# Performance work log

Hardware: AMD Instinct MI355X
Metric: run time of the kernel (lower is better)

Reference implementation:

```python
import jax, jax.numpy as jnp
import numpy as np

LEVELS = 16
FEATURES = 2
HASHMAP_SIZE = 524288
BASE_RES = 16
PER_LEVEL_SCALE = 1.3819

_P1, _P2, _P3 = np.uint32(73856093), np.uint32(19349663), np.uint32(83492791)
# 8 trilinear corner offsets, bit order (x, y, z)
_OFFSETS = np.array([[ox, oy, oz] for ox in (0, 1) for oy in (0, 1) for oz in (0, 1)], dtype=np.int32)


def setup_inputs() -> dict:
    key = jax.random.key(0)
    kx, kt = jax.random.split(key)
    x = jax.random.uniform(kx, (2000000, 3), dtype=jnp.float32)
    tables = jax.random.normal(kt, (LEVELS, HASHMAP_SIZE, FEATURES), dtype=jnp.float32) * 0.01
    return {"x": x, "tables": tables}


def _hash_coords(corners_u32):
    # corners_u32: [N, 8, 3] uint32; spatial hash with uint32 wraparound.
    h = (corners_u32[..., 0] * _P1) ^ (corners_u32[..., 1] * _P2) ^ (corners_u32[..., 2] * _P3)
    return (h % np.uint32(HASHMAP_SIZE)).astype(jnp.int32)  # [N, 8]


def _encode(x, tables):
    offsets_i = jnp.asarray(_OFFSETS)                 # [8, 3] int32
    offsets_f = offsets_i.astype(x.dtype)             # [8, 3]
    embeds = []
    for l in range(LEVELS):
        res = int(BASE_RES * PER_LEVEL_SCALE ** l)
        pos = x * res                                  # [N, 3]
        pos_floor = jnp.floor(pos)
        w = pos - pos_floor                            # [N, 3] trilinear weights
        base = pos_floor.astype(jnp.int32)             # non-negative (x in [0,1])
        corners = (base[:, None, :] + offsets_i).astype(jnp.uint32)  # [N, 8, 3]
        idx = _hash_coords(corners)                    # [N, 8]
        vals = tables[l][idx]                          # [N, 8, F] gather
        # weight per corner = prod over axes of (w if offset else 1-w)
        wgt = jnp.prod(offsets_f * w[:, None, :] + (1.0 - offsets_f) * (1.0 - w[:, None, :]), axis=-1)  # [N, 8]
        embeds.append(jnp.einsum('nc,ncf->nf', wgt, vals))  # [N, F]
    return jnp.concatenate(embeds, axis=-1)           # [N, LEVELS*F]


def reference(x, tables):
    return _encode(x, tables)
```

## Files before the change

### kernel.cpp

```cpp
#include <hip/hip_runtime.h>
#include <stdint.h>

#define LEVELS 16
#define FEAT 2
#define TABLE_SIZE 524288
#define TMASK (TABLE_SIZE - 1)

typedef float f32x2 __attribute__((ext_vector_type(2)));
typedef float f32x4 __attribute__((ext_vector_type(4)));
typedef float f32x4u __attribute__((ext_vector_type(4), aligned(8)));

__device__ __constant__ int kRes[LEVELS] = {
    16, 22, 30, 42, 58, 80, 111, 153, 212, 294, 406, 561, 775, 1072, 1481, 2047
};

#define P1 73856093u
#define P2 19349663u
#define P3 83492791u

#define D0 17
#define N0 4913
#define D1 23
#define N1 12167
#define D2 31
#define N2 29791
#define D3 43
#define N3 79507
#define D4 59
#define N4 205379
#define NDENSE (N0 + N1 + N2 + N3 + N4)

__global__ __launch_bounds__(256) void remap_kernel(
    const float* __restrict__ tables,
    f32x2* __restrict__ dense)
{
    const int d = blockIdx.x * 256 + threadIdx.x;
    if (d >= NDENSE) return;
    int l, D, rel;
    if (d < N0)                          { l = 0; D = D0; rel = d; }
    else if (d < N0 + N1)                { l = 1; D = D1; rel = d - N0; }
    else if (d < N0 + N1 + N2)           { l = 2; D = D2; rel = d - N0 - N1; }
    else if (d < N0 + N1 + N2 + N3)      { l = 3; D = D3; rel = d - N0 - N1 - N2; }
    else                                 { l = 4; D = D4; rel = d - N0 - N1 - N2 - N3; }
    const uint32_t bx = rel / (D * D);
    const uint32_t r  = rel - bx * (D * D);
    const uint32_t by = r / D;
    const uint32_t bz = r - by * D;
    const uint32_t slot = ((bx * P1) ^ (by * P2) ^ (bz * P3)) & TMASK;
    const f32x2* __restrict__ tab = reinterpret_cast<const f32x2*>(tables) + (size_t)l * TABLE_SIZE;
    dense[d] = tab[slot];
}

__device__ __constant__ int   kDD[5]    = { D0, D1, D2, D3, D4 };
__device__ __constant__ int   kDOff[5]  = { 0, N0, N0 + N1, N0 + N1 + N2, N0 + N1 + N2 + N3 };
__device__ __constant__ float kDRes[5]  = { 16.0f, 22.0f, 30.0f, 42.0f, 58.0f };

__global__ __launch_bounds__(256) void encode_dense_kernel(
    const float* __restrict__ x,
    const f32x2* __restrict__ dense,
    f32x2* __restrict__ ws,
    int n, int nb)
{
    const int lsel = blockIdx.x / nb;
    const int blk  = blockIdx.x - lsel * nb;
    const int t    = threadIdx.x;
    const int p0   = blk * 1024;

    __shared__ float sx[1024 * 3];
    const long long total3 = (long long)n * 3;
    const long long gbase  = (long long)p0 * 3;
#pragma unroll
    for (int k = 0; k < 12; ++k) {
        long long g = gbase + k * 256 + t;
        sx[k * 256 + t] = (g < total3) ? __builtin_nontemporal_load(x + g) : 0.0f;
    }
    __syncthreads();

    const int   D    = kDD[lsel];
    const int   DD   = D * D;
    const float resf = kDRes[lsel];
    const f32x2* __restrict__ tabd = dense + kDOff[lsel];

    int   base[4];
    float wxa[4], wya[4], wza[4];
#pragma unroll
    for (int s = 0; s < 4; ++s) {
        const int tp = s * 256 + t;
        const float fx = sx[3 * tp + 0] * resf;
        const float fy = sx[3 * tp + 1] * resf;
        const float fz = sx[3 * tp + 2] * resf;
        const float flx = floorf(fx), fly = floorf(fy), flz = floorf(fz);
        wxa[s] = fx - flx; wya[s] = fy - fly; wza[s] = fz - flz;
        base[s] = ((int)flx * D + (int)fly) * D + (int)flz;
    }

    f32x4u v[4][4];
#pragma unroll
    for (int s = 0; s < 4; ++s)
#pragma unroll
        for (int p = 0; p < 4; ++p) {
            const int off = ((p & 2) ? DD : 0) + ((p & 1) ? D : 0);
            v[s][p] = *reinterpret_cast<const f32x4u*>(tabd + base[s] + off);
        }
    __builtin_amdgcn_sched_barrier(0);

#pragma unroll
    for (int s = 0; s < 4; ++s) {
        const float wx = wxa[s], wy = wya[s], wz = wza[s];
        const float ux = 1.0f - wx, uy = 1.0f - wy, uz = 1.0f - wz;
        float f0 = 0.0f, f1 = 0.0f;
#pragma unroll
        for (int p = 0; p < 4; ++p) {
            const float wxy = ((p & 2) ? wx : ux) * ((p & 1) ? wy : uy);
            f0 = fmaf(wxy, fmaf(uz, v[s][p].x, wz * v[s][p].z), f0);
            f1 = fmaf(wxy, fmaf(uz, v[s][p].y, wz * v[s][p].w), f1);
        }
        const int i = p0 + s * 256 + t;
        if (i < n) {
            f32x2 r; r.x = f0; r.y = f1;
            __builtin_nontemporal_store(r, ws + (size_t)lsel * n + i);
        }
    }
}

__global__ __launch_bounds__(256) void encode_level_kernel(
    const float* __restrict__ x,
    const float* __restrict__ tables,
    f32x2* __restrict__ ws,
    int n, int nb)
{
    const int l   = 5 + blockIdx.x / nb;
    const int blk = blockIdx.x - (l - 5) * nb;
    const int t   = threadIdx.x;
    const int p0  = blk * 1024;

    __shared__ float sx[1024 * 3];
    const long long total3 = (long long)n * 3;
    const long long gbase  = (long long)p0 * 3;
#pragma unroll
    for (int k = 0; k < 12; ++k) {
        long long g = gbase + k * 256 + t;
        sx[k * 256 + t] = (g < total3) ? __builtin_nontemporal_load(x + g) : 0.0f;
    }
    __syncthreads();

    const float resf = (float)kRes[l];
    const f32x2* __restrict__ tab = reinterpret_cast<const f32x2*>(tables) + (size_t)l * TABLE_SIZE;

    uint32_t idx[4][8];
    float    wxa[4], wya[4], wza[4];
#pragma unroll
    for (int s = 0; s < 4; ++s) {
        const int tp = s * 256 + t;
        const float fx = sx[3 * tp + 0] * resf;
        const float fy = sx[3 * tp + 1] * resf;
        const float fz = sx[3 * tp + 2] * resf;
        const float flx = floorf(fx), fly = floorf(fy), flz = floorf(fz);
        wxa[s] = fx - flx; wya[s] = fy - fly; wza[s] = fz - flz;
        const uint32_t hx0 = (uint32_t)(int)flx * P1, hx1 = hx0 + P1;
        const uint32_t hy0 = (uint32_t)(int)fly * P2, hy1 = hy0 + P2;
        const uint32_t hz0 = (uint32_t)(int)flz * P3, hz1 = hz0 + P3;
#pragma unroll
        for (int c = 0; c < 8; ++c) {
            const uint32_t hx = (c & 4) ? hx1 : hx0;
            const uint32_t hy = (c & 2) ? hy1 : hy0;
            const uint32_t hz = (c & 1) ? hz1 : hz0;
            idx[s][c] = (hx ^ hy ^ hz) & TMASK;
        }
    }

    f32x2 v[4][8];
#pragma unroll
    for (int s = 0; s < 4; ++s)
#pragma unroll
        for (int c = 0; c < 8; ++c)
            v[s][c] = tab[idx[s][c]];
    __builtin_amdgcn_sched_barrier(0);

#pragma unroll
    for (int s = 0; s < 4; ++s) {
        const float wx = wxa[s], wy = wya[s], wz = wza[s];
        const float ux = 1.0f - wx, uy = 1.0f - wy, uz = 1.0f - wz;
        float f0 = 0.0f, f1 = 0.0f;
#pragma unroll
        for (int c = 0; c < 8; ++c) {
            const float w = ((c & 4) ? wx : ux) * ((c & 2) ? wy : uy) * ((c & 1) ? wz : uz);
            f0 = fmaf(w, v[s][c].x, f0);
            f1 = fmaf(w, v[s][c].y, f1);
        }
        const int i = p0 + s * 256 + t;
        if (i < n) {
            f32x2 r; r.x = f0; r.y = f1;
            __builtin_nontemporal_store(r, ws + (size_t)l * n + i);
        }
    }
}

__global__ __launch_bounds__(256) void transpose_kernel(
    const f32x2* __restrict__ ws,
    float* __restrict__ out,
    int n)
{
    __shared__ float s[256 * 33];
    const int t  = threadIdx.x;
    const int p0 = blockIdx.x * 256;
    const int m  = min(256, n - p0);

    if (t < m) {
#pragma unroll
        for (int l = 0; l < LEVELS; ++l) {
            const f32x2 e = __builtin_nontemporal_load(ws + (size_t)l * n + p0 + t);
            s[t * 33 + 2 * l + 0] = e.x;
            s[t * 33 + 2 * l + 1] = e.y;
        }
    }
    __syncthreads();

    const int nchunk = m * 8;
    f32x4* __restrict__ o4 = reinterpret_cast<f32x4*>(out) + (size_t)p0 * 8;
#pragma unroll
    for (int j = 0; j < 8; ++j) {
        const int cl = j * 256 + t;
        if (cl < nchunk) {
            const int p = cl >> 3, ch = cl & 7;
            f32x4 q;
            q.x = s[p * 33 + ch * 4 + 0];
            q.y = s[p * 33 + ch * 4 + 1];
            q.z = s[p * 33 + ch * 4 + 2];
            q.w = s[p * 33 + ch * 4 + 3];
            __builtin_nontemporal_store(q, o4 + cl);
        }
    }
}

__global__ __launch_bounds__(256) void hashgrid_enc_kernel(
    const float* __restrict__ x,
    const float* __restrict__ tables,
    float* __restrict__ out,
    int n)
{
    __shared__ float sx[256 * 3];
    const int t = threadIdx.x;
    const int block0 = blockIdx.x * 256;
    const long long total3 = (long long)n * 3;
    const long long gbase = (long long)block0 * 3;
#pragma unroll
    for (int k = 0; k < 3; ++k) {
        long long g = gbase + k * 256 + t;
        sx[k * 256 + t] = (g < total3) ? x[g] : 0.0f;
    }
    __syncthreads();
    const int i = block0 + t;
    if (i >= n) return;
    const float px = sx[3 * t + 0];
    const float py = sx[3 * t + 1];
    const float pz = sx[3 * t + 2];
    float outv[2 * LEVELS];
#pragma unroll
    for (int l = 0; l < LEVELS; ++l) {
        const float resf = (float)kRes[l];
        const float fx = px * resf, fy = py * resf, fz = pz * resf;
        const float flx = floorf(fx), fly = floorf(fy), flz = floorf(fz);
        const float wx = fx - flx, wy = fy - fly, wz = fz - flz;
        const float ux = 1.0f - wx, uy = 1.0f - wy, uz = 1.0f - wz;
        const uint32_t hx0 = (uint32_t)(int)flx * P1, hx1 = hx0 + P1;
        const uint32_t hy0 = (uint32_t)(int)fly * P2, hy1 = hy0 + P2;
        const uint32_t hz0 = (uint32_t)(int)flz * P3, hz1 = hz0 + P3;
        const float* __restrict__ tab = tables + (size_t)l * (TABLE_SIZE * FEAT);
        float f0 = 0.0f, f1 = 0.0f;
#pragma unroll
        for (int c = 0; c < 8; ++c) {
            const uint32_t hx = (c & 4) ? hx1 : hx0;
            const uint32_t hy = (c & 2) ? hy1 : hy0;
            const uint32_t hz = (c & 1) ? hz1 : hz0;
            const uint32_t idx = (hx ^ hy ^ hz) & TMASK;
            const float2 v = *reinterpret_cast<const float2*>(tab + (size_t)idx * FEAT);
            const float w = ((c & 4) ? wx : ux) * ((c & 2) ? wy : uy) * ((c & 1) ? wz : uz);
            f0 = fmaf(w, v.x, f0);
            f1 = fmaf(w, v.y, f1);
        }
        outv[2 * l + 0] = f0;
        outv[2 * l + 1] = f1;
    }
    float4* __restrict__ o4 = reinterpret_cast<float4*>(out + (size_t)i * (2 * LEVELS));
#pragma unroll
    for (int k = 0; k < 8; ++k) {
        o4[k] = make_float4(outv[4 * k + 0], outv[4 * k + 1],
                            outv[4 * k + 2], outv[4 * k + 3]);
    }
}

extern "C" void kernel_launch(void* const* d_in, const int* in_sizes, int n_in,
                              void* d_out, int out_size, void* d_ws, size_t ws_size,
                              hipStream_t stream) {
    const float* x = (const float*)d_in[0];
    const float* tables = (const float*)d_in[1];
    float* out = (float*)d_out;
    const int n = in_sizes[0] / 3;

    const size_t ws_elems  = (size_t)LEVELS * (size_t)n;
    const size_t ws_needed = (ws_elems + NDENSE + 2) * sizeof(f32x2);
    if (ws_size >= ws_needed) {
        f32x2* ws    = (f32x2*)d_ws;
        f32x2* dense = ws + ws_elems;

        hipLaunchKernelGGL(remap_kernel, dim3((NDENSE + 255) / 256), dim3(256), 0, stream,
                           tables, dense);

        const int nb1024 = (n + 1023) / 1024;
        hipLaunchKernelGGL(encode_dense_kernel, dim3(nb1024 * 5), dim3(256), 0, stream,
                           x, dense, ws, n, nb1024);
        hipLaunchKernelGGL(encode_level_kernel, dim3(nb1024 * 11), dim3(256), 0, stream,
                           x, tables, ws, n, nb1024);

        const int nb256 = (n + 255) / 256;
        hipLaunchKernelGGL(transpose_kernel, dim3(nb256), dim3(256), 0, stream,
                           ws, out, n);
    } else {
        const int nb = (n + 255) / 256;
        hipLaunchKernelGGL(hashgrid_enc_kernel, dim3(nb), dim3(256), 0, stream,
                           x, tables, out, n);
    }
}
```

Measured before the change: 1.126 ms.

## Extend dense remap to level 5 and loop dense levels per block

Level 5 (res 80, 81^3 cells) is now also remapped into a dense, collision-free layout, so its hashed 8-corner gather becomes four paired 16-byte loads when the workspace has room. The dense encode kernel now loads each point block once and loops over all dense levels instead of launching one block per level. Points per block drop from 1024 to 512 in both encode kernels, the explicit sched barriers are removed, and corner weights are precomputed before the gathers. The cost is a larger remap pass (about 531K extra entries) and lower memory-level parallelism per thread.

Result: faster. 1.048 ms (-6.9%).

```diff
diff --git a/kernel.cpp b/kernel.cpp
--- a/kernel.cpp
+++ b/kernel.cpp
@@ -28,20 +28,29 @@
 #define N3 79507
 #define D4 59
 #define N4 205379
-#define NDENSE (N0 + N1 + N2 + N3 + N4)
+#define D5 81
+#define N5 531441
+#define NDENSE5 (N0 + N1 + N2 + N3 + N4)
+#define NDENSE6 (NDENSE5 + N5)
+
+__device__ __constant__ int   kDD[6]   = { D0, D1, D2, D3, D4, D5 };
+__device__ __constant__ int   kDOff[6] = { 0, N0, N0+N1, N0+N1+N2, N0+N1+N2+N3, NDENSE5 };
+__device__ __constant__ float kDRes[6] = { 16.0f, 22.0f, 30.0f, 42.0f, 58.0f, 80.0f };
+__device__ __constant__ int   kDCum[7] = { 0, N0, N0+N1, N0+N1+N2, N0+N1+N2+N3, NDENSE5, NDENSE6 };
 
 __global__ __launch_bounds__(256) void remap_kernel(
     const float* __restrict__ tables,
-    f32x2* __restrict__ dense)
+    f32x2* __restrict__ dense,
+    int total)
 {
     const int d = blockIdx.x * 256 + threadIdx.x;
-    if (d >= NDENSE) return;
-    int l, D, rel;
-    if (d < N0)                          { l = 0; D = D0; rel = d; }
-    else if (d < N0 + N1)                { l = 1; D = D1; rel = d - N0; }
-    else if (d < N0 + N1 + N2)           { l = 2; D = D2; rel = d - N0 - N1; }
-    else if (d < N0 + N1 + N2 + N3)      { l = 3; D = D3; rel = d - N0 - N1 - N2; }
-    else                                 { l = 4; D = D4; rel = d - N0 - N1 - N2 - N3; }
+    if (d >= total) return;
+    int l = 0;
+#pragma unroll
+    for (int k = 1; k < 6; ++k)
+        if (d >= kDCum[k]) l = k;
+    const int D   = kDD[l];
+    const int rel = d - kDCum[l];
     const uint32_t bx = rel / (D * D);
     const uint32_t r  = rel - bx * (D * D);
     const uint32_t by = r / D;
@@ -51,112 +60,112 @@
     dense[d] = tab[slot];
 }
 
-__device__ __constant__ int   kDD[5]    = { D0, D1, D2, D3, D4 };
-__device__ __constant__ int   kDOff[5]  = { 0, N0, N0 + N1, N0 + N1 + N2, N0 + N1 + N2 + N3 };
-__device__ __constant__ float kDRes[5]  = { 16.0f, 22.0f, 30.0f, 42.0f, 58.0f };
-
 __global__ __launch_bounds__(256) void encode_dense_kernel(
     const float* __restrict__ x,
     const f32x2* __restrict__ dense,
     f32x2* __restrict__ ws,
-    int n, int nb)
-{
-    const int lsel = blockIdx.x / nb;
-    const int blk  = blockIdx.x - lsel * nb;
-    const int t    = threadIdx.x;
-    const int p0   = blk * 1024;
-
-    __shared__ float sx[1024 * 3];
+    int n, int ndlev)
+{
+    const int blk = blockIdx.x;
+    const int t   = threadIdx.x;
+    const int p0  = blk * 512;
+
+    __shared__ float sx[512 * 3];
     const long long total3 = (long long)n * 3;
     const long long gbase  = (long long)p0 * 3;
 #pragma unroll
-    for (int k = 0; k < 12; ++k) {
+    for (int k = 0; k < 6; ++k) {
         long long g = gbase + k * 256 + t;
         sx[k * 256 + t] = (g < total3) ? __builtin_nontemporal_load(x + g) : 0.0f;
     }
     __syncthreads();
 
-    const int   D    = kDD[lsel];
-    const int   DD   = D * D;
-    const float resf = kDRes[lsel];
-    const f32x2* __restrict__ tabd = dense + kDOff[lsel];
-
-    int   base[4];
-    float wxa[4], wya[4], wza[4];
-#pragma unroll
-    for (int s = 0; s < 4; ++s) {
+    const float px[2] = { sx[3 * t + 0],          sx[3 * (t + 256) + 0] };
+    const float py[2] = { sx[3 * t + 1],          sx[3 * (t + 256) + 1] };
+    const float pz[2] = { sx[3 * t + 2],          sx[3 * (t + 256) + 2] };
+
+    for (int l = 0; l < ndlev; ++l) {
+        const int   D    = kDD[l];
+        const int   DD   = D * D;
+        const float resf = kDRes[l];
+        const f32x2* __restrict__ tabd = dense + kDOff[l];
+
+        int   base[2];
+        float wxa[2], wya[2], wza[2];
+#pragma unroll
+        for (int s = 0; s < 2; ++s) {
+            const float fx = px[s] * resf;
+            const float fy = py[s] * resf;
+            const float fz = pz[s] * resf;
+            const float flx = floorf(fx), fly = floorf(fy), flz = floorf(fz);
+            wxa[s] = fx - flx; wya[s] = fy - fly; wza[s] = fz - flz;
+            base[s] = ((int)flx * D + (int)fly) * D + (int)flz;
+        }
+
+        f32x4u v[2][4];
+#pragma unroll
+        for (int s = 0; s < 2; ++s)
+#pragma unroll
+            for (int p = 0; p < 4; ++p) {
+                const int off = ((p & 2) ? DD : 0) + ((p & 1) ? D : 0);
+                v[s][p] = *reinterpret_cast<const f32x4u*>(tabd + base[s] + off);
+            }
+
+#pragma unroll
+        for (int s = 0; s < 2; ++s) {
+            const float wx = wxa[s], wy = wya[s], wz = wza[s];
+            const float ux = 1.0f - wx, uy = 1.0f - wy, uz = 1.0f - wz;
+            float f0 = 0.0f, f1 = 0.0f;
+#pragma unroll
+            for (int p = 0; p < 4; ++p) {
+                const float wxy = ((p & 2) ? wx : ux) * ((p & 1) ? wy : uy);
+                f0 = fmaf(wxy, fmaf(uz, v[s][p].x, wz * v[s][p].z), f0);
+                f1 = fmaf(wxy, fmaf(uz, v[s][p].y, wz * v[s][p].w), f1);
+            }
+            const int i = p0 + s * 256 + t;
+            if (i < n) {
+                f32x2 r; r.x = f0; r.y = f1;
+                __builtin_nontemporal_store(r, ws + (size_t)l * n + i);
+            }
+        }
+    }
+}
+
+__global__ __launch_bounds__(256) void encode_level_kernel(
+    const float* __restrict__ x,
+    const float* __restrict__ tables,
+    f32x2* __restrict__ ws,
+    int n, int nb, int l0)
+{
+    const int l   = l0 + blockIdx.x / nb;
+    const int blk = blockIdx.x - (l - l0) * nb;
+    const int t   = threadIdx.x;
+    const int p0  = blk * 512;
+
+    __shared__ float sx[512 * 3];
+    const long long total3 = (long long)n * 3;
+    const long long gbase  = (long long)p0 * 3;
+#pragma unroll
+    for (int k = 0; k < 6; ++k) {
+        long long g = gbase + k * 256 + t;
+        sx[k * 256 + t] = (g < total3) ? __builtin_nontemporal_load(x + g) : 0.0f;
+    }
+    __syncthreads();
+
+    const float resf = (float)kRes[l];
+    const f32x2* __restrict__ tab = reinterpret_cast<const f32x2*>(tables) + (size_t)l * TABLE_SIZE;
+
+    uint32_t idx[2][8];
+    float    wgt[2][8];
+#pragma unroll
+    for (int s = 0; s < 2; ++s) {
         const int tp = s * 256 + t;
         const float fx = sx[3 * tp + 0] * resf;
         const float fy = sx[3 * tp + 1] * resf;
         const float fz = sx[3 * tp + 2] * resf;
         const float flx = floorf(fx), fly = floorf(fy), flz = floorf(fz);
-        wxa[s] = fx - flx; wya[s] = fy - fly; wza[s] = fz - flz;
-        base[s] = ((int)flx * D + (int)fly) * D + (int)flz;
-    }
-
-    f32x4u v[4][4];
-#pragma unroll
-    for (int s = 0; s < 4; ++s)
-#pragma unroll
-        for (int p = 0; p < 4; ++p) {
-            const int off = ((p & 2) ? DD : 0) + ((p & 1) ? D : 0);
-            v[s][p] = *reinterpret_cast<const f32x4u*>(tabd + base[s] + off);
-        }
-    __builtin_amdgcn_sched_barrier(0);
-
-#pragma unroll
-    for (int s = 0; s < 4; ++s) {
-        const float wx = wxa[s], wy = wya[s], wz = wza[s];
+        const float wx = fx - flx, wy = fy - fly, wz = fz - flz;
         const float ux = 1.0f - wx, uy = 1.0f - wy, uz = 1.0f - wz;
-        float f0 = 0.0f, f1 = 0.0f;
-#pragma unroll
-        for (int p = 0; p < 4; ++p) {
-            const float wxy = ((p & 2) ? wx : ux) * ((p & 1) ? wy : uy);
-            f0 = fmaf(wxy, fmaf(uz, v[s][p].x, wz * v[s][p].z), f0);
-            f1 = fmaf(wxy, fmaf(uz, v[s][p].y, wz * v[s][p].w), f1);
-        }
-        const int i = p0 + s * 256 + t;
-        if (i < n) {
-            f32x2 r; r.x = f0; r.y = f1;
-            __builtin_nontemporal_store(r, ws + (size_t)lsel * n + i);
-        }
-    }
-}
-
-__global__ __launch_bounds__(256) void encode_level_kernel(
-    const float* __restrict__ x,
-    const float* __restrict__ tables,
-    f32x2* __restrict__ ws,
-    int n, int nb)
-{
-    const int l   = 5 + blockIdx.x / nb;
-    const int blk = blockIdx.x - (l - 5) * nb;
-    const int t   = threadIdx.x;
-    const int p0  = blk * 1024;
-
-    __shared__ float sx[1024 * 3];
-    const long long total3 = (long long)n * 3;
-    const long long gbase  = (long long)p0 * 3;
-#pragma unroll
-    for (int k = 0; k < 12; ++k) {
-        long long g = gbase + k * 256 + t;
-        sx[k * 256 + t] = (g < total3) ? __builtin_nontemporal_load(x + g) : 0.0f;
-    }
-    __syncthreads();
-
-    const float resf = (float)kRes[l];
-    const f32x2* __restrict__ tab = reinterpret_cast<const f32x2*>(tables) + (size_t)l * TABLE_SIZE;
-
-    uint32_t idx[4][8];
-    float    wxa[4], wya[4], wza[4];
-#pragma unroll
-    for (int s = 0; s < 4; ++s) {
-        const int tp = s * 256 + t;
-        const float fx = sx[3 * tp + 0] * resf;
-        const float fy = sx[3 * tp + 1] * resf;
-        const float fz = sx[3 * tp + 2] * resf;
-        const float flx = floorf(fx), fly = floorf(fy), flz = floorf(fz);
-        wxa[s] = fx - flx; wya[s] = fy - fly; wza[s] = fz - flz;
         const uint32_t hx0 = (uint32_t)(int)flx * P1, hx1 = hx0 + P1;
         const uint32_t hy0 = (uint32_t)(int)fly * P2, hy1 = hy0 + P2;
         const uint32_t hz0 = (uint32_t)(int)flz * P3, hz1 = hz0 + P3;
@@ -166,27 +175,24 @@
             const uint32_t hy = (c & 2) ? hy1 : hy0;
             const uint32_t hz = (c & 1) ? hz1 : hz0;
             idx[s][c] = (hx ^ hy ^ hz) & TMASK;
-        }
-    }
-
-    f32x2 v[4][8];
-#pragma unroll
-    for (int s = 0; s < 4; ++s)
+            wgt[s][c] = ((c & 4) ? wx : ux) * ((c & 2) ? wy : uy) * ((c & 1) ? wz : uz);
+        }
+    }
+
+    f32x2 v[2][8];
+#pragma unroll
+    for (int s = 0; s < 2; ++s)
 #pragma unroll
         for (int c = 0; c < 8; ++c)
             v[s][c] = tab[idx[s][c]];
-    __builtin_amdgcn_sched_barrier(0);
-
-#pragma unroll
-    for (int s = 0; s < 4; ++s) {
-        const float wx = wxa[s], wy = wya[s], wz = wza[s];
-        const float ux = 1.0f - wx, uy = 1.0f - wy, uz = 1.0f - wz;
+
+#pragma unroll
+    for (int s = 0; s < 2; ++s) {
         float f0 = 0.0f, f1 = 0.0f;
 #pragma unroll
         for (int c = 0; c < 8; ++c) {
-            const float w = ((c & 4) ? wx : ux) * ((c & 2) ? wy : uy) * ((c & 1) ? wz : uz);
-            f0 = fmaf(w, v[s][c].x, f0);
-            f1 = fmaf(w, v[s][c].y, f1);
+            f0 = fmaf(wgt[s][c], v[s][c].x, f0);
+            f1 = fmaf(wgt[s][c], v[s][c].y, f1);
         }
         const int i = p0 + s * 256 + t;
         if (i < n) {
@@ -298,20 +304,26 @@
     float* out = (float*)d_out;
     const int n = in_sizes[0] / 3;
 
-    const size_t ws_elems  = (size_t)LEVELS * (size_t)n;
-    const size_t ws_needed = (ws_elems + NDENSE + 2) * sizeof(f32x2);
-    if (ws_size >= ws_needed) {
+    const size_t ws_elems = (size_t)LEVELS * (size_t)n;
+    const size_t needA = (ws_elems + NDENSE6 + 2) * sizeof(f32x2);
+    const size_t needB = (ws_elems + NDENSE5 + 2) * sizeof(f32x2);
+
+    if (ws_size >= needB) {
+        const int  planA  = (ws_size >= needA);
+        const int  ndlev  = planA ? 6 : 5;
+        const int  l0     = planA ? 6 : 5;
+        const int  total  = planA ? NDENSE6 : NDENSE5;
         f32x2* ws    = (f32x2*)d_ws;
         f32x2* dense = ws + ws_elems;
 
-        hipLaunchKernelGGL(remap_kernel, dim3((NDENSE + 255) / 256), dim3(256), 0, stream,
-                           tables, dense);
-
-        const int nb1024 = (n + 1023) / 1024;
-        hipLaunchKernelGGL(encode_dense_kernel, dim3(nb1024 * 5), dim3(256), 0, stream,
-                           x, dense, ws, n, nb1024);
-        hipLaunchKernelGGL(encode_level_kernel, dim3(nb1024 * 11), dim3(256), 0, stream,
-                           x, tables, ws, n, nb1024);
+        hipLaunchKernelGGL(remap_kernel, dim3((total + 255) / 256), dim3(256), 0, stream,
+                           tables, dense, total);
+
+        const int nb512 = (n + 511) / 512;
+        hipLaunchKernelGGL(encode_dense_kernel, dim3(nb512), dim3(256), 0, stream,
+                           x, dense, ws, n, ndlev);
+        hipLaunchKernelGGL(encode_level_kernel, dim3(nb512 * (LEVELS - l0)), dim3(256), 0, stream,
+                           x, tables, ws, n, nb512, l0);
 
         const int nb256 = (n + 255) / 256;
         hipLaunchKernelGGL(transpose_kernel, dim3(nb256), dim3(256), 0, stream,
```
